# Performance work log

Hardware: AMD Instinct MI355X
Metric: run time of the kernel (lower is better)

Reference implementation:

```python
import jax, jax.numpy as jnp
import numpy as np

N_NODES = 100000
N_EDGES = 800000
D = 256
OUT = 1

def _glorot(key, shape):
    fan_in, fan_out = shape[1], shape[0]
    lim = np.sqrt(6.0 / (fan_in + fan_out)).astype(np.float32)
    return jax.random.uniform(key, shape, jnp.float32, -lim, lim)

def setup_inputs() -> dict:
    key = jax.random.key(0)
    ks = jax.random.split(key, 12)
    x = jax.random.normal(ks[0], (N_NODES, D), jnp.float32)
    edge_index = jax.random.randint(ks[1], (2, N_EDGES), 0, N_NODES, jnp.int64)
    return {
        "x": x,
        "edge_index": edge_index,
        # SAGEConv: lin_l acts on aggregated neighbors (has bias), lin_r on root (no bias)
        "W_l": _glorot(ks[2], (256, D)),
        "b_l": jnp.zeros((256,), jnp.float32),
        "W_r": _glorot(ks[3], (256, D)),
        # MLP
        "W1": _glorot(ks[4], (128, 256)),
        "b1": jnp.zeros((128,), jnp.float32),
        "W2": _glorot(ks[5], (32, 128)),
        "b2": jnp.zeros((32,), jnp.float32),
        "W3": _glorot(ks[6], (OUT, 32)),
        "b3": jnp.zeros((OUT,), jnp.float32),
    }

def reference(x, edge_index, W_l, b_l, W_r, W1, b1, W2, b2, W3, b3):
    src, dst = edge_index[0], edge_index[1]
    # mean aggregation of neighbor (source) features at destination nodes
    msg = x[src]                                            # [E, D]
    agg = jax.ops.segment_sum(msg, dst, num_segments=N_NODES)   # [N, D]
    cnt = jax.ops.segment_sum(jnp.ones((edge_index.shape[1],), x.dtype), dst,
                              num_segments=N_NODES)          # [N]
    mean = agg / jnp.maximum(cnt, 1.0)[:, None]
    # SAGEConv: lin_l(mean_neigh) + lin_r(x)
    conv = mean @ W_l.T + b_l + x @ W_r.T                   # [N, 256]
    out = jax.nn.relu(conv)
    h = out + x                                              # residual
    h = jax.nn.relu(h @ W1.T + b1)
    h = jax.nn.relu(h @ W2.T + b2)
    return h @ W3.T + b3                                     # [N, OUT]
```

## Files before the change

kernel.cpp:

```cpp
#include <hip/hip_runtime.h>
#include <cstddef>

#define NN 100000
#define NE 800000
#define DD 256
#define CAP 40

typedef unsigned short u16;
typedef __bf16 bf8_t __attribute__((ext_vector_type(8)));
typedef float f32x4 __attribute__((ext_vector_type(4)));
typedef u16 u16x8 __attribute__((ext_vector_type(8)));

__device__ __forceinline__ float bf2f(u16 u) {
    union { unsigned int i; float f; } v; v.i = ((unsigned int)u) << 16; return v.f;
}
__device__ __forceinline__ u16 f2bf(float f) {
    union { float f; unsigned int i; } v; v.f = f;
    unsigned int x = v.i;
    unsigned int r = (x + 0x7FFFu + ((x >> 16) & 1u)) >> 16;
    return (u16)r;
}

__device__ __forceinline__ void bar_lds() {
    asm volatile("s_waitcnt lgkmcnt(0)" ::: "memory");
    __builtin_amdgcn_s_barrier();
    asm volatile("" ::: "memory");
}

__global__ void GNNActor_23192823398472_kernel() {}

__global__ void k_prep(const u16* __restrict__ x, const int* __restrict__ ei,
                       int* __restrict__ flags, int4* __restrict__ z4, int nz4) {
    int i = blockIdx.x * blockDim.x + threadIdx.x;
    if (i < nz4) z4[i] = (int4){0, 0, 0, 0};
    if (blockIdx.x == 0 && threadIdx.x < 64) {
        int lane = threadIdx.x;
        int big = 0;
        for (int k = lane; k < 4096; k += 64) {
            u16 u = x[k];
            if (((u >> 7) & 0xFF) >= 140) ++big;
        }
        #pragma unroll
        for (int off = 32; off; off >>= 1) big += __shfl_down(big, off, 64);
        int bad = 0;
        for (int k = lane; k < 128; k += 64) bad |= (ei[2 * k + 1] != 0) ? 1 : 0;
        unsigned long long anybad = __ballot(bad);
        if (lane == 0) {
            flags[0] = (big > 64) ? 1 : 0;
            flags[1] = anybad ? 0 : 1;
        }
    }
}

__device__ __forceinline__ float ldwf(const void* p, int i, int f32) {
    return f32 ? ((const float*)p)[i] : bf2f(((const u16*)p)[i]);
}
__global__ void k_pack(const void* __restrict__ Wl, const void* __restrict__ Wr,
                       const void* __restrict__ W1, const void* __restrict__ W2,
                       const void* __restrict__ W3, const void* __restrict__ bl,
                       const void* __restrict__ b1, const void* __restrict__ b2,
                       const void* __restrict__ b3, u16* __restrict__ pk,
                       float* __restrict__ pb, const int* __restrict__ flags) {
    int id = blockIdx.x * blockDim.x + threadIdx.x;
    int f32 = flags[0];
    if (id < 16384) {
        int lr = id & 15, lq = (id >> 4) & 3, c = (id >> 6) & 15, ctg = id >> 10;
        int n = ctg * 16 + lr;
        int k = (c & 7) * 32 + lq * 8;
        const void* W = (c < 8) ? Wl : Wr;
        u16x8 o;
        #pragma unroll
        for (int j = 0; j < 8; ++j) o[j] = f2bf(ldwf(W, n * DD + k + j, f32));
        *(u16x8*)&pk[id * 8] = o;
    } else if (id < 20480) {
        int id2 = id - 16384;
        int lr = id2 & 15, lq = (id2 >> 4) & 3, c = (id2 >> 6) & 7, wv = id2 >> 9;
        int n = wv * 16 + lr;
        u16x8 o;
        #pragma unroll
        for (int j = 0; j < 8; ++j) o[j] = f2bf(ldwf(W1, n * DD + c * 32 + lq * 8 + j, f32));
        *(u16x8*)&pk[131072 + id2 * 8] = o;
    } else if (id < 20992) {
        int id2 = id - 20480;
        int lr = id2 & 15, lq = (id2 >> 4) & 3, c = (id2 >> 6) & 3, wv = id2 >> 8;
        int n = wv * 16 + lr;
        u16x8 o;
        #pragma unroll
        for (int j = 0; j < 8; ++j) o[j] = f2bf(ldwf(W2, n * 128 + c * 32 + lq * 8 + j, f32));
        *(u16x8*)&pk[163840 + id2 * 8] = o;
    } else if (id < 21441) {
        int j = id - 20992;
        float v;
        if (j < 256)      v = ldwf(bl, j, f32);
        else if (j < 384) v = ldwf(b1, j - 256, f32);
        else if (j < 416) v = ldwf(b2, j - 384, f32);
        else if (j == 416) v = ldwf(b3, 0, f32);
        else              v = ldwf(W3, j - 417, f32);
        pb[j] = v;
    }
}

__global__ void k_scatter(const int* __restrict__ ei, int* __restrict__ cnt_i,
                          int* __restrict__ elist, const int* __restrict__ flags) {
    int e0 = (blockIdx.x * blockDim.x + threadIdx.x) * 4;
    if (e0 >= NE) return;
    int d0, d1, d2, d3, s0, s1, s2, s3;
    if (flags[1]) {
        int4 a = *(const int4*)&ei[2 * NE + 2 * e0];
        int4 b = *(const int4*)&ei[2 * NE + 2 * e0 + 4];
        d0 = a.x; d1 = a.z; d2 = b.x; d3 = b.z;
        int4 p = *(const int4*)&ei[2 * e0];
        int4 q = *(const int4*)&ei[2 * e0 + 4];
        s0 = p.x; s1 = p.z; s2 = q.x; s3 = q.z;
    } else {
        int4 a = *(const int4*)&ei[NE + e0];
        d0 = a.x; d1 = a.y; d2 = a.z; d3 = a.w;
        int4 p = *(const int4*)&ei[e0];
        s0 = p.x; s1 = p.y; s2 = p.z; s3 = p.w;
    }
    int p0 = atomicAdd(&cnt_i[d0], 1); if (p0 < CAP) elist[d0 * CAP + p0] = s0;
    int p1 = atomicAdd(&cnt_i[d1], 1); if (p1 < CAP) elist[d1 * CAP + p1] = s1;
    int p2 = atomicAdd(&cnt_i[d2], 1); if (p2 < CAP) elist[d2 * CAP + p2] = s2;
    int p3 = atomicAdd(&cnt_i[d3], 1); if (p3 < CAP) elist[d3 * CAP + p3] = s3;
}

template <int F32>
__device__ __forceinline__ void gather_body(const int* __restrict__ cnt_i,
                                            const int* __restrict__ elist,
                                            const void* __restrict__ xv,
                                            u16* __restrict__ meanb) {
    int wv = threadIdx.x >> 6, lane = threadIdx.x & 63;
    int n = blockIdx.x * 4 + wv;
    int cnt = cnt_i[n];
    int m = cnt < CAP ? cnt : CAP;
    float a0 = 0.f, a1 = 0.f, a2 = 0.f, a3 = 0.f;
    if (m > 0) {
        int j = (lane < m) ? lane : 0;
        int idxl = elist[n * CAP + j];
        for (int b = 0; b < m; b += 8) {
            int nb = m - b; if (nb > 8) nb = 8;
            ushort4 u[8]; float4 f[8]; float msk[8];
            #pragma unroll
            for (int g = 0; g < 8; ++g) {
                int src = __shfl(idxl, b + g, 64);
                msk[g] = (g < nb) ? 1.f : 0.f;
                if (F32) f[g] = *(const float4*)((const float*)xv + (size_t)src * DD + (lane << 2));
                else     u[g] = *(const ushort4*)((const u16*)xv + (size_t)src * DD + (lane << 2));
            }
            #pragma unroll
            for (int g = 0; g < 8; ++g) {
                if (F32) {
                    a0 = fmaf(msk[g], f[g].x, a0); a1 = fmaf(msk[g], f[g].y, a1);
                    a2 = fmaf(msk[g], f[g].z, a2); a3 = fmaf(msk[g], f[g].w, a3);
                } else {
                    a0 = fmaf(msk[g], bf2f(u[g].x), a0); a1 = fmaf(msk[g], bf2f(u[g].y), a1);
                    a2 = fmaf(msk[g], bf2f(u[g].z), a2); a3 = fmaf(msk[g], bf2f(u[g].w), a3);
                }
            }
        }
    }
    float inv = 1.f / fmaxf((float)cnt, 1.f);
    ushort4 o;
    o.x = f2bf(a0 * inv); o.y = f2bf(a1 * inv);
    o.z = f2bf(a2 * inv); o.w = f2bf(a3 * inv);
    *(ushort4*)&meanb[(size_t)n * DD + (lane << 2)] = o;
}

__launch_bounds__(256)
__global__ void k_gather(const int* __restrict__ cnt_i, const int* __restrict__ elist,
                         const void* __restrict__ xv, u16* __restrict__ meanb,
                         const int* __restrict__ flags) {
    if (flags[0]) gather_body<1>(cnt_i, elist, xv, meanb);
    else          gather_body<0>(cnt_i, elist, xv, meanb);
}

#define SMS 264
#define SH1 136
#define SH2 40

template <int F32>
__device__ __forceinline__ void mm_body(
        const u16* __restrict__ meanb, const void* __restrict__ xv,
        const u16* __restrict__ pk, const float* __restrict__ pb,
        void* __restrict__ outv, char* smem) {
    u16* s_mean = (u16*)smem;
    u16* s_x    = (u16*)(smem + 16896);
    u16* s_h    = (u16*)smem;
    u16* s_h1   = (u16*)(smem + 16896);
    u16* s_h2   = (u16*)smem;

    int t = threadIdx.x;
    int node0 = blockIdx.x * 32;
    int wv = t >> 6, lane = t & 63;
    int lq = lane >> 4, lr = lane & 15;
    int fo = lq * 128 + lr * 8;

    const u16* pk1 = pk + 131072;
    const u16* pk2 = pk + 163840;
    int ctg0 = wv * 2, ctg1 = ctg0 + 1;

    #define LWC(ctg, c) (*(const bf8_t*)&pk[((ctg) * 16 + (c)) * 512 + fo])

    bf8_t w0[16], w1[16];
    #pragma unroll
    for (int c = 0; c < 4; ++c) { w0[c] = LWC(ctg0, c); w1[c] = LWC(ctg1, c); }

    {
        int i0 = t, i1 = t + 512;
        int r0 = i0 >> 5, k0 = (i0 & 31) << 3;
        int r1 = i1 >> 5, k1 = (i1 & 31) << 3;
        u16x8 m0 = *(const u16x8*)&meanb[(size_t)(node0 + r0) * DD + k0];
        u16x8 m1 = *(const u16x8*)&meanb[(size_t)(node0 + r1) * DD + k1];
        u16x8 x0, x1;
        if (F32) {
            const float* p0 = (const float*)xv + (size_t)(node0 + r0) * DD + k0;
            const float* p1 = (const float*)xv + (size_t)(node0 + r1) * DD + k1;
            float4 fa = *(const float4*)p0, fb = *(const float4*)(p0 + 4);
            float4 fc = *(const float4*)p1, fd = *(const float4*)(p1 + 4);
            x0[0]=f2bf(fa.x); x0[1]=f2bf(fa.y); x0[2]=f2bf(fa.z); x0[3]=f2bf(fa.w);
            x0[4]=f2bf(fb.x); x0[5]=f2bf(fb.y); x0[6]=f2bf(fb.z); x0[7]=f2bf(fb.w);
            x1[0]=f2bf(fc.x); x1[1]=f2bf(fc.y); x1[2]=f2bf(fc.z); x1[3]=f2bf(fc.w);
            x1[4]=f2bf(fd.x); x1[5]=f2bf(fd.y); x1[6]=f2bf(fd.z); x1[7]=f2bf(fd.w);
        } else {
            x0 = *(const u16x8*)((const u16*)xv + (size_t)(node0 + r0) * DD + k0);
            x1 = *(const u16x8*)((const u16*)xv + (size_t)(node0 + r1) * DD + k1);
        }
        *(u16x8*)&s_mean[r0 * SMS + k0] = m0;
        *(u16x8*)&s_mean[r1 * SMS + k1] = m1;
        *(u16x8*)&s_x[r0 * SMS + k0] = x0;
        *(u16x8*)&s_x[r1 * SMS + k1] = x1;
    }
    bar_lds();

    f32x4 acc00 = (f32x4){0.f,0.f,0.f,0.f}, acc10 = (f32x4){0.f,0.f,0.f,0.f};
    f32x4 acc01 = (f32x4){0.f,0.f,0.f,0.f}, acc11 = (f32x4){0.f,0.f,0.f,0.f};

    #pragma unroll
    for (int c = 0; c < 16; ++c) {
        if (c < 12) { w0[c + 4] = LWC(ctg0, c + 4); w1[c + 4] = LWC(ctg1, c + 4); }
        const u16* ab = (c < 8) ? s_mean : s_x;
        int co = (c & 7) * 32 + lq * 8;
        bf8_t a0 = *(const bf8_t*)&ab[lr * SMS + co];
        bf8_t a1 = *(const bf8_t*)&ab[(16 + lr) * SMS + co];
        acc00 = __builtin_amdgcn_mfma_f32_16x16x32_bf16(a0, w0[c], acc00, 0, 0, 0);
        acc10 = __builtin_amdgcn_mfma_f32_16x16x32_bf16(a1, w0[c], acc10, 0, 0, 0);
        acc01 = __builtin_amdgcn_mfma_f32_16x16x32_bf16(a0, w1[c], acc01, 0, 0, 0);
        acc11 = __builtin_amdgcn_mfma_f32_16x16x32_bf16(a1, w1[c], acc11, 0, 0, 0);
    }

    bf8_t v1[8];
    #pragma unroll
    for (int c = 0; c < 8; ++c) v1[c] = *(const bf8_t*)&pk1[(wv * 8 + c) * 512 + fo];

    bar_lds();

    #pragma unroll
    for (int ct = 0; ct < 2; ++ct) {
        int n = (wv * 2 + ct) * 16 + lr;
        float bb = pb[n];
        const f32x4* ac0 = ct ? &acc01 : &acc00;
        const f32x4* ac1 = ct ? &acc11 : &acc10;
        #pragma unroll
        for (int i = 0; i < 4; ++i) {
            int m0 = lq * 4 + i;
            s_h[m0 * SMS + n] = f2bf(fmaxf((*ac0)[i] + bb, 0.f) + bf2f(s_x[m0 * SMS + n]));
            int m1 = 16 + lq * 4 + i;
            s_h[m1 * SMS + n] = f2bf(fmaxf((*ac1)[i] + bb, 0.f) + bf2f(s_x[m1 * SMS + n]));
        }
    }
    bar_lds();

    {
        f32x4 a1c0 = (f32x4){0.f,0.f,0.f,0.f}, a1c1 = (f32x4){0.f,0.f,0.f,0.f};
        int n = wv * 16 + lr;
        #pragma unroll
        for (int c = 0; c < 8; ++c) {
            bf8_t a0 = *(const bf8_t*)&s_h[lr * SMS + c * 32 + lq * 8];
            bf8_t a1 = *(const bf8_t*)&s_h[(16 + lr) * SMS + c * 32 + lq * 8];
            a1c0 = __builtin_amdgcn_mfma_f32_16x16x32_bf16(a0, v1[c], a1c0, 0, 0, 0);
            a1c1 = __builtin_amdgcn_mfma_f32_16x16x32_bf16(a1, v1[c], a1c1, 0, 0, 0);
        }
        bf8_t v2[4];
        if (wv < 2) {
            #pragma unroll
            for (int c = 0; c < 4; ++c) v2[c] = *(const bf8_t*)&pk2[(wv * 4 + c) * 512 + fo];
        }
        float bb = pb[256 + n];
        #pragma unroll
        for (int i = 0; i < 4; ++i) {
            int m0 = lq * 4 + i;
            s_h1[m0 * SH1 + n] = f2bf(fmaxf(a1c0[i] + bb, 0.f));
            int m1 = 16 + lq * 4 + i;
            s_h1[m1 * SH1 + n] = f2bf(fmaxf(a1c1[i] + bb, 0.f));
        }
        bar_lds();

        if (wv < 2) {
            f32x4 a2c0 = (f32x4){0.f,0.f,0.f,0.f}, a2c1 = (f32x4){0.f,0.f,0.f,0.f};
            #pragma unroll
            for (int c = 0; c < 4; ++c) {
                bf8_t a0 = *(const bf8_t*)&s_h1[lr * SH1 + c * 32 + lq * 8];
                bf8_t a1 = *(const bf8_t*)&s_h1[(16 + lr) * SH1 + c * 32 + lq * 8];
                a2c0 = __builtin_amdgcn_mfma_f32_16x16x32_bf16(a0, v2[c], a2c0, 0, 0, 0);
                a2c1 = __builtin_amdgcn_mfma_f32_16x16x32_bf16(a1, v2[c], a2c1, 0, 0, 0);
            }
            float bb2 = pb[384 + n];
            #pragma unroll
            for (int i = 0; i < 4; ++i) {
                int m0 = lq * 4 + i;
                s_h2[m0 * SH2 + n] = f2bf(fmaxf(a2c0[i] + bb2, 0.f));
                int m1 = 16 + lq * 4 + i;
                s_h2[m1 * SH2 + n] = f2bf(fmaxf(a2c1[i] + bb2, 0.f));
            }
        }
    }
    bar_lds();

    if (t < 32) {
        float a3 = pb[416];
        #pragma unroll
        for (int k = 0; k < 32; ++k)
            a3 += bf2f(s_h2[t * SH2 + k]) * pb[417 + k];
        if (F32) ((float*)outv)[node0 + t] = a3;
        else     ((u16*)outv)[node0 + t]   = f2bf(a3);
    }
    #undef LWC
}

__launch_bounds__(512, 4)
__global__ void k_mm(const u16* __restrict__ meanb, const void* __restrict__ xv,
                     const u16* __restrict__ pk, const float* __restrict__ pb,
                     void* __restrict__ outv, const int* __restrict__ flags) {
    __shared__ __align__(16) char smem[33792];
    if (flags[0]) mm_body<1>(meanb, xv, pk, pb, outv, smem);
    else          mm_body<0>(meanb, xv, pk, pb, outv, smem);
}

extern "C" void kernel_launch(void* const* d_in, const int* in_sizes, int n_in,
                              void* d_out, int out_size, void* d_ws, size_t ws_size,
                              hipStream_t stream) {
    const u16* x  = (const u16*)d_in[0];
    const int* ei = (const int*)d_in[1];
    const void* Wl = d_in[2];
    const void* bl = d_in[3];
    const void* Wr = d_in[4];
    const void* W1 = d_in[5];
    const void* b1 = d_in[6];
    const void* W2 = d_in[7];
    const void* b2 = d_in[8];
    const void* W3 = d_in[9];
    const void* b3 = d_in[10];

    u16* meanb = (u16*)d_ws;
    int* flags = (int*)(meanb + (size_t)NN * DD);
    int* cnt_i = flags + 256;
    int* elist = cnt_i + NN;
    u16* pk    = (u16*)(elist + (size_t)NN * CAP);
    float* pb  = (float*)(pk + 167936);

    k_prep<<<(NN / 4 + 255) / 256, 256, 0, stream>>>(x, ei, flags, (int4*)cnt_i, NN / 4);
    k_pack<<<84, 256, 0, stream>>>(Wl, Wr, W1, W2, W3, bl, b1, b2, b3, pk, pb, flags);
    k_scatter<<<(NE / 4 + 255) / 256, 256, 0, stream>>>(ei, cnt_i, elist, flags);
    k_gather<<<NN / 4, 256, 0, stream>>>(cnt_i, elist, (const void*)x, meanb, flags);
    k_mm<<<NN / 32, 512, 0, stream>>>(meanb, (const void*)x, pk, pb, d_out, flags);
}
```

Before: 376.3 us.

## Merge prep and pack kernels; restructure gather with LDS indices and 16-byte loads

```diff
diff --git a/kernel.cpp b/kernel.cpp
--- a/kernel.cpp
+++ b/kernel.cpp
@@ -29,11 +29,43 @@
 
 __global__ void GNNActor_23192823398472_kernel() {}
 
+__device__ __forceinline__ float ldwf(const void* p, int i, int f32) {
+    return f32 ? ((const float*)p)[i] : bf2f(((const u16*)p)[i]);
+}
+
 __global__ void k_prep(const u16* __restrict__ x, const int* __restrict__ ei,
-                       int* __restrict__ flags, int4* __restrict__ z4, int nz4) {
-    int i = blockIdx.x * blockDim.x + threadIdx.x;
-    if (i < nz4) z4[i] = (int4){0, 0, 0, 0};
-    if (blockIdx.x == 0 && threadIdx.x < 64) {
+                       int* __restrict__ flags, int4* __restrict__ z4, int nz4,
+                       const void* __restrict__ Wl, const void* __restrict__ Wr,
+                       const void* __restrict__ W1, const void* __restrict__ W2,
+                       const void* __restrict__ W3, const void* __restrict__ bl,
+                       const void* __restrict__ b1, const void* __restrict__ b2,
+                       const void* __restrict__ b3, u16* __restrict__ pk,
+                       float* __restrict__ pb) {
+    int nzb = (nz4 + 255) / 256;
+    if ((int)blockIdx.x < nzb) {
+        int i = blockIdx.x * 256 + threadIdx.x;
+        if (i < nz4) z4[i] = (int4){0, 0, 0, 0};
+        if (blockIdx.x == 0 && threadIdx.x < 64) {
+            int lane = threadIdx.x;
+            int big = 0;
+            for (int k = lane; k < 4096; k += 64) {
+                u16 u = x[k];
+                if (((u >> 7) & 0xFF) >= 140) ++big;
+            }
+            #pragma unroll
+            for (int off = 32; off; off >>= 1) big += __shfl_down(big, off, 64);
+            int bad = 0;
+            for (int k = lane; k < 128; k += 64) bad |= (ei[2 * k + 1] != 0) ? 1 : 0;
+            unsigned long long anybad = __ballot(bad);
+            if (lane == 0) {
+                flags[0] = (big > 64) ? 1 : 0;
+                flags[1] = anybad ? 0 : 1;
+            }
+        }
+        return;
+    }
+    __shared__ int s_f32;
+    if (threadIdx.x < 64) {
         int lane = threadIdx.x;
         int big = 0;
         for (int k = lane; k < 4096; k += 64) {
@@ -42,27 +74,11 @@
         }
         #pragma unroll
         for (int off = 32; off; off >>= 1) big += __shfl_down(big, off, 64);
-        int bad = 0;
-        for (int k = lane; k < 128; k += 64) bad |= (ei[2 * k + 1] != 0) ? 1 : 0;
-        unsigned long long anybad = __ballot(bad);
-        if (lane == 0) {
-            flags[0] = (big > 64) ? 1 : 0;
-            flags[1] = anybad ? 0 : 1;
-        }
-    }
-}
-
-__device__ __forceinline__ float ldwf(const void* p, int i, int f32) {
-    return f32 ? ((const float*)p)[i] : bf2f(((const u16*)p)[i]);
-}
-__global__ void k_pack(const void* __restrict__ Wl, const void* __restrict__ Wr,
-                       const void* __restrict__ W1, const void* __restrict__ W2,
-                       const void* __restrict__ W3, const void* __restrict__ bl,
-                       const void* __restrict__ b1, const void* __restrict__ b2,
-                       const void* __restrict__ b3, u16* __restrict__ pk,
-                       float* __restrict__ pb, const int* __restrict__ flags) {
-    int id = blockIdx.x * blockDim.x + threadIdx.x;
-    int f32 = flags[0];
+        if (lane == 0) s_f32 = (big > 64) ? 1 : 0;
+    }
+    __syncthreads();
+    int f32 = s_f32;
+    int id = (blockIdx.x - nzb) * 256 + threadIdx.x;
     if (id < 16384) {
         int lr = id & 15, lq = (id >> 4) & 3, c = (id >> 6) & 15, ctg = id >> 10;
         int n = ctg * 16 + lr;
@@ -128,50 +144,74 @@
 __device__ __forceinline__ void gather_body(const int* __restrict__ cnt_i,
                                             const int* __restrict__ elist,
                                             const void* __restrict__ xv,
-                                            u16* __restrict__ meanb) {
-    int wv = threadIdx.x >> 6, lane = threadIdx.x & 63;
-    int n = blockIdx.x * 4 + wv;
-    int cnt = cnt_i[n];
-    int m = cnt < CAP ? cnt : CAP;
-    float a0 = 0.f, a1 = 0.f, a2 = 0.f, a3 = 0.f;
-    if (m > 0) {
-        int j = (lane < m) ? lane : 0;
-        int idxl = elist[n * CAP + j];
-        for (int b = 0; b < m; b += 8) {
-            int nb = m - b; if (nb > 8) nb = 8;
-            ushort4 u[8]; float4 f[8]; float msk[8];
+                                            u16* __restrict__ meanb,
+                                            int* s_idx, int* s_cnt) {
+    int t = threadIdx.x;
+    int node0 = blockIdx.x * 16;
+    if (t < 160) ((int4*)s_idx)[t] = ((const int4*)&elist[node0 * CAP])[t];
+    if (t < 16) s_cnt[t] = cnt_i[node0 + t];
+    __syncthreads();
+
+    int wv = t >> 6, lane = t & 63, half = lane >> 5, li = lane & 31;
+    for (int q = 0; q < 4; ++q) {
+        int n = wv * 4 + q;
+        int cnt = s_cnt[n];
+        int m = cnt < CAP ? cnt : CAP;
+        float a0=0.f,a1=0.f,a2=0.f,a3=0.f,a4=0.f,a5=0.f,a6=0.f,a7=0.f;
+        for (int b = 0; b < m; b += 16) {
+            u16x8 u[8]; float4 fA[8], fB[8]; float msk[8];
             #pragma unroll
             for (int g = 0; g < 8; ++g) {
-                int src = __shfl(idxl, b + g, 64);
-                msk[g] = (g < nb) ? 1.f : 0.f;
-                if (F32) f[g] = *(const float4*)((const float*)xv + (size_t)src * DD + (lane << 2));
-                else     u[g] = *(const ushort4*)((const u16*)xv + (size_t)src * DD + (lane << 2));
+                int j = b + g * 2 + half;
+                int ok = j < m;
+                int jj = ok ? j : 0;
+                msk[g] = ok ? 1.f : 0.f;
+                int src = s_idx[n * CAP + jj];
+                if (F32) {
+                    const float* p = (const float*)xv + (size_t)src * DD + li * 8;
+                    fA[g] = *(const float4*)p;
+                    fB[g] = *(const float4*)(p + 4);
+                } else {
+                    u[g] = *(const u16x8*)((const u16*)xv + (size_t)src * DD + li * 8);
+                }
             }
             #pragma unroll
             for (int g = 0; g < 8; ++g) {
                 if (F32) {
-                    a0 = fmaf(msk[g], f[g].x, a0); a1 = fmaf(msk[g], f[g].y, a1);
-                    a2 = fmaf(msk[g], f[g].z, a2); a3 = fmaf(msk[g], f[g].w, a3);
+                    a0 = fmaf(msk[g], fA[g].x, a0); a1 = fmaf(msk[g], fA[g].y, a1);
+                    a2 = fmaf(msk[g], fA[g].z, a2); a3 = fmaf(msk[g], fA[g].w, a3);
+                    a4 = fmaf(msk[g], fB[g].x, a4); a5 = fmaf(msk[g], fB[g].y, a5);
+                    a6 = fmaf(msk[g], fB[g].z, a6); a7 = fmaf(msk[g], fB[g].w, a7);
                 } else {
-                    a0 = fmaf(msk[g], bf2f(u[g].x), a0); a1 = fmaf(msk[g], bf2f(u[g].y), a1);
-                    a2 = fmaf(msk[g], bf2f(u[g].z), a2); a3 = fmaf(msk[g], bf2f(u[g].w), a3);
+                    a0 = fmaf(msk[g], bf2f(u[g][0]), a0); a1 = fmaf(msk[g], bf2f(u[g][1]), a1);
+                    a2 = fmaf(msk[g], bf2f(u[g][2]), a2); a3 = fmaf(msk[g], bf2f(u[g][3]), a3);
+                    a4 = fmaf(msk[g], bf2f(u[g][4]), a4); a5 = fmaf(msk[g], bf2f(u[g][5]), a5);
+                    a6 = fmaf(msk[g], bf2f(u[g][6]), a6); a7 = fmaf(msk[g], bf2f(u[g][7]), a7);
                 }
             }
         }
-    }
-    float inv = 1.f / fmaxf((float)cnt, 1.f);
-    ushort4 o;
-    o.x = f2bf(a0 * inv); o.y = f2bf(a1 * inv);
-    o.z = f2bf(a2 * inv); o.w = f2bf(a3 * inv);
-    *(ushort4*)&meanb[(size_t)n * DD + (lane << 2)] = o;
+        a0 += __shfl_xor(a0, 32, 64); a1 += __shfl_xor(a1, 32, 64);
+        a2 += __shfl_xor(a2, 32, 64); a3 += __shfl_xor(a3, 32, 64);
+        a4 += __shfl_xor(a4, 32, 64); a5 += __shfl_xor(a5, 32, 64);
+        a6 += __shfl_xor(a6, 32, 64); a7 += __shfl_xor(a7, 32, 64);
+        if (lane < 32) {
+            float inv = 1.f / fmaxf((float)cnt, 1.f);
+            u16x8 o;
+            o[0]=f2bf(a0*inv); o[1]=f2bf(a1*inv); o[2]=f2bf(a2*inv); o[3]=f2bf(a3*inv);
+            o[4]=f2bf(a4*inv); o[5]=f2bf(a5*inv); o[6]=f2bf(a6*inv); o[7]=f2bf(a7*inv);
+            *(u16x8*)&meanb[(size_t)(node0 + n) * DD + li * 8] = o;
+        }
+    }
 }
 
 __launch_bounds__(256)
 __global__ void k_gather(const int* __restrict__ cnt_i, const int* __restrict__ elist,
                          const void* __restrict__ xv, u16* __restrict__ meanb,
                          const int* __restrict__ flags) {
-    if (flags[0]) gather_body<1>(cnt_i, elist, xv, meanb);
-    else          gather_body<0>(cnt_i, elist, xv, meanb);
+    __shared__ int s_idx[16 * CAP];
+    __shared__ int s_cnt[16];
+    if (flags[0]) gather_body<1>(cnt_i, elist, xv, meanb, s_idx, s_cnt);
+    else          gather_body<0>(cnt_i, elist, xv, meanb, s_idx, s_cnt);
 }
 
 #define SMS 264
@@ -358,9 +398,11 @@
     u16* pk    = (u16*)(elist + (size_t)NN * CAP);
     float* pb  = (float*)(pk + 167936);
 
-    k_prep<<<(NN / 4 + 255) / 256, 256, 0, stream>>>(x, ei, flags, (int4*)cnt_i, NN / 4);
-    k_pack<<<84, 256, 0, stream>>>(Wl, Wr, W1, W2, W3, bl, b1, b2, b3, pk, pb, flags);
+    int nz4 = NN / 4;
+    int nzb = (nz4 + 255) / 256;
+    k_prep<<<nzb + 84, 256, 0, stream>>>(x, ei, flags, (int4*)cnt_i, nz4,
+                                         Wl, Wr, W1, W2, W3, bl, b1, b2, b3, pk, pb);
     k_scatter<<<(NE / 4 + 255) / 256, 256, 0, stream>>>(ei, cnt_i, elist, flags);
-    k_gather<<<NN / 4, 256, 0, stream>>>(cnt_i, elist, (const void*)x, meanb, flags);
+    k_gather<<<NN / 16, 256, 0, stream>>>(cnt_i, elist, (const void*)x, meanb, flags);
     k_mm<<<NN / 32, 512, 0, stream>>>(meanb, (const void*)x, pk, pb, d_out, flags);
 }
```

New measurement: 388.4 us. +3.2%, slower.
